# Kernel tuning notes

Hardware: AMD Instinct MI355X
Metric: run time of the kernel (lower is better)

The kernel has to match this reference:

```python
import jax, jax.numpy as jnp
import numpy as np

EMBED = 768
HEADS = 12
HEAD_DIM = EMBED // HEADS
DEPTH = 4
PATCH = 16
GRID = 32  # 512 / 16
MLP_DIM = 4 * EMBED
LN_EPS = 1e-5


def layer_norm(x, w, b):
    m = jnp.mean(x, axis=-1, keepdims=True)
    v = jnp.mean(jnp.square(x - m), axis=-1, keepdims=True)
    return (x - m) * jax.lax.rsqrt(v + LN_EPS) * w + b


def sam_attention(x, qkv_w, qkv_b, proj_w, proj_b, rel_pos_h, rel_pos_w):
    B, H, W, C = x.shape
    N = H * W
    scale = HEAD_DIM ** -0.5
    qkv = x.reshape(B, N, C) @ qkv_w + qkv_b  # (B, N, 3C)
    qkv = qkv.reshape(B, N, 3, HEADS, HEAD_DIM).transpose(2, 0, 3, 1, 4)
    qkv = qkv.reshape(3, B * HEADS, N, HEAD_DIM)
    q, k, v = qkv[0], qkv[1], qkv[2]
    attn = jnp.einsum('bqc,bkc->bqk', q * scale, k)  # (B*nh, N, N)
    # decomposed relative position (q_size == k_size, table already max_rel_dist)
    idx_h = jnp.arange(H)[:, None] - jnp.arange(H)[None, :] + (H - 1)
    idx_w = jnp.arange(W)[:, None] - jnp.arange(W)[None, :] + (W - 1)
    Rh = rel_pos_h[idx_h]  # (H, H, hd)
    Rw = rel_pos_w[idx_w]  # (W, W, hd)
    r_q = q.reshape(B * HEADS, H, W, HEAD_DIM)
    rel_h = jnp.einsum('bhwc,hkc->bhwk', r_q, Rh)
    rel_w = jnp.einsum('bhwc,wkc->bhwk', r_q, Rw)
    attn = (attn.reshape(B * HEADS, H, W, H, W)
            + rel_h[:, :, :, :, None]
            + rel_w[:, :, :, None, :]).reshape(B * HEADS, N, N)
    attn = jax.nn.softmax(attn, axis=-1)
    out = (attn @ v).reshape(B, HEADS, H, W, HEAD_DIM)
    out = out.transpose(0, 2, 3, 1, 4).reshape(B, H, W, C)
    return out @ proj_w + proj_b


def setup_inputs() -> dict:
    key = jax.random.key(0)
    ks = jax.random.split(key, 20)
    s = lambda k, shape, sc=0.02: jax.random.normal(k, shape, jnp.float32) * sc
    inp = {
        'x': jax.random.normal(ks[0], (4, 3, 512, 512), jnp.float32),
        'conv_w': s(ks[1], (EMBED, 3, PATCH, PATCH)),
        'conv_b': jnp.zeros((EMBED,), jnp.float32),
        'pos_embed': s(ks[2], (1, GRID, GRID, EMBED)),
        'ln1_w': jnp.ones((DEPTH, EMBED), jnp.float32),
        'ln1_b': jnp.zeros((DEPTH, EMBED), jnp.float32),
        'qkv_w': s(ks[3], (DEPTH, EMBED, 3 * EMBED)),
        'qkv_b': jnp.zeros((DEPTH, 3 * EMBED), jnp.float32),
        'proj_w': s(ks[4], (DEPTH, EMBED, EMBED)),
        'proj_b': jnp.zeros((DEPTH, EMBED), jnp.float32),
        'rel_pos_h': s(ks[5], (DEPTH, 2 * GRID - 1, HEAD_DIM)),
        'rel_pos_w': s(ks[6], (DEPTH, 2 * GRID - 1, HEAD_DIM)),
        'ln2_w': jnp.ones((DEPTH, EMBED), jnp.float32),
        'ln2_b': jnp.zeros((DEPTH, EMBED), jnp.float32),
        'fc1_w': s(ks[7], (DEPTH, EMBED, MLP_DIM)),
        'fc1_b': jnp.zeros((DEPTH, MLP_DIM), jnp.float32),
        'fc2_w': s(ks[8], (DEPTH, MLP_DIM, EMBED)),
        'fc2_b': jnp.zeros((DEPTH, EMBED), jnp.float32),
    }
    return inp


def reference(x, conv_w, conv_b, pos_embed, ln1_w, ln1_b, qkv_w, qkv_b,
              proj_w, proj_b, rel_pos_h, rel_pos_w, ln2_w, ln2_b,
              fc1_w, fc1_b, fc2_w, fc2_b):
    # patch embed: conv stride=patch, then NCHW -> NHWC
    h = jax.lax.conv_general_dilated(
        x, conv_w, window_strides=(PATCH, PATCH), padding='VALID',
        dimension_numbers=('NCHW', 'OIHW', 'NCHW'))
    h = h.transpose(0, 2, 3, 1) + conv_b  # (B, 32, 32, 768)
    h = h + pos_embed
    for i in range(DEPTH):
        a = sam_attention(layer_norm(h, ln1_w[i], ln1_b[i]),
                          qkv_w[i], qkv_b[i], proj_w[i], proj_b[i],
                          rel_pos_h[i], rel_pos_w[i])
        h = h + a
        m = layer_norm(h, ln2_w[i], ln2_b[i])
        m = jax.nn.gelu(m @ fc1_w[i] + fc1_b[i], approximate=False) @ fc2_w[i] + fc2_b[i]
        h = h + m
    return h
```

## Files before the change

### kernel.cpp

```cpp
#include <hip/hip_runtime.h>
#include <hip/hip_bf16.h>
#include <math.h>
#include <stdint.h>

#define EMBED 768
#define NTOK  1024
#define BATCH 4
#define NHEAD 12
#define HD    64
#define MLPD  3072
#define M_ROWS 4096

typedef __attribute__((ext_vector_type(8))) short short8;
typedef __attribute__((ext_vector_type(4))) float floatx4;

__device__ __forceinline__ float b2f(__hip_bfloat16 v) { return __bfloat162float(v); }

__device__ __forceinline__ void gld_lds16(const void* g, void* l) {
    __builtin_amdgcn_global_load_lds(
        (const __attribute__((address_space(1))) uint32_t*)g,
        (__attribute__((address_space(3))) uint32_t*)l, 16, 0, 0);
}

__device__ __forceinline__ int swz(int row, int c) { return row*64 + (((c) ^ (row & 7)) << 3); }

__global__ __launch_bounds__(256)
void im2col(const float* __restrict__ x, __hip_bfloat16* __restrict__ A)
{
    int p  = blockIdx.x;
    int b  = p >> 10;
    int n  = p & 1023;
    int gh = n >> 5, gw = n & 31;
    int tid = threadIdx.x;
    for (int i = tid; i < 768; i += 256) {
        int ci = i >> 8, r = i & 255, kh = r >> 4, kw = r & 15;
        A[(size_t)p*768 + i] = __float2bfloat16(
            x[(((size_t)b*3 + ci)*512 + (gh*16 + kh))*512 + gw*16 + kw]);
    }
}

__global__ __launch_bounds__(256)
void cvt_bf16(const float* __restrict__ in, __hip_bfloat16* __restrict__ out, int n)
{
    int i = blockIdx.x*256 + threadIdx.x;
    if (i < n) out[i] = __float2bfloat16(in[i]);
}

__global__ __launch_bounds__(256)
void layernorm_bf16(const float* __restrict__ in,
                    const float* __restrict__ w,
                    const float* __restrict__ b,
                    __hip_bfloat16* __restrict__ out)
{
    int row = blockIdx.x;
    const float* xr = in + (size_t)row*768;
    int tid = threadIdx.x;
    float v0 = xr[tid], v1 = xr[tid+256], v2 = xr[tid+512];
    float s = v0+v1+v2, ss = v0*v0+v1*v1+v2*v2;
    __shared__ float rs[256], rss[256];
    rs[tid] = s; rss[tid] = ss; __syncthreads();
    for (int o = 128; o > 0; o >>= 1) {
        if (tid < o) { rs[tid] += rs[tid+o]; rss[tid] += rss[tid+o]; }
        __syncthreads();
    }
    float mean = rs[0] * (1.f/768.f);
    float var  = rss[0] * (1.f/768.f) - mean*mean;
    float inv  = rsqrtf(var + 1e-5f);
    out[(size_t)row*768 + tid]     = __float2bfloat16((v0-mean)*inv*w[tid]     + b[tid]);
    out[(size_t)row*768 + tid+256] = __float2bfloat16((v1-mean)*inv*w[tid+256] + b[tid+256]);
    out[(size_t)row*768 + tid+512] = __float2bfloat16((v2-mean)*inv*w[tid+512] + b[tid+512]);
}

__global__ __launch_bounds__(256)
void resum_ln(float* __restrict__ h,
              const float* __restrict__ p0, const float* __restrict__ p1,
              const float* __restrict__ bias,
              const float* __restrict__ w, const float* __restrict__ b,
              __hip_bfloat16* __restrict__ out)
{
    int row = blockIdx.x;
    int tid = threadIdx.x;
    size_t base = (size_t)row*768;
    float v[3];
    float s = 0.f, ss = 0.f;
    #pragma unroll
    for (int e = 0; e < 3; ++e) {
        int i = tid + e*256;
        float val = h[base+i] + p0[base+i] + p1[base+i] + bias[i];
        h[base+i] = val;
        v[e] = val; s += val; ss += val*val;
    }
    __shared__ float rs[256], rss[256];
    rs[tid] = s; rss[tid] = ss; __syncthreads();
    for (int o = 128; o > 0; o >>= 1) {
        if (tid < o) { rs[tid] += rs[tid+o]; rss[tid] += rss[tid+o]; }
        __syncthreads();
    }
    float mean = rs[0] * (1.f/768.f);
    float var  = rss[0] * (1.f/768.f) - mean*mean;
    float inv  = rsqrtf(var + 1e-5f);
    #pragma unroll
    for (int e = 0; e < 3; ++e) {
        int i = tid + e*256;
        out[base+i] = __float2bfloat16((v[e]-mean)*inv*w[i] + b[i]);
    }
}

__global__ __launch_bounds__(256)
void resum_out(const float* __restrict__ h,
               const float* __restrict__ p0, const float* __restrict__ p1,
               const float* __restrict__ bias,
               float* __restrict__ out)
{
    int i = blockIdx.x*256 + threadIdx.x;
    out[i] = h[i] + p0[i] + p1[i] + bias[i % 768];
}

__global__ __launch_bounds__(256)
void prep_weights(const float* __restrict__ qkv_w,  const float* __restrict__ proj_w,
                  const float* __restrict__ fc1_w,  const float* __restrict__ fc2_w,
                  __hip_bfloat16* __restrict__ qkv_wt, __hip_bfloat16* __restrict__ proj_wt,
                  __hip_bfloat16* __restrict__ fc1_wt, __hip_bfloat16* __restrict__ fc2_wt)
{
    int id = blockIdx.x;
    const float* src; __hip_bfloat16* dst; int K, N, bx, by;
    if (id < 1728)      {            src = qkv_w;  dst = qkv_wt;  K = 768;  N = 2304; bx = id % 72; by = id / 72; }
    else if (id < 2304) { id -= 1728; src = proj_w; dst = proj_wt; K = 768;  N = 768;  bx = id % 24; by = id / 24; }
    else if (id < 4608) { id -= 2304; src = fc1_w;  dst = fc1_wt;  K = 768;  N = 3072; bx = id % 96; by = id / 96; }
    else                { id -= 4608; src = fc2_w;  dst = fc2_wt;  K = 3072; N = 768;  bx = id % 24; by = id / 24; }

    __shared__ float t[32][33];
    int n0 = bx*32, k0 = by*32;
    int tx = threadIdx.x & 31, ty = threadIdx.x >> 5;
    #pragma unroll
    for (int r = 0; r < 4; ++r) {
        int row = ty + r*8;
        t[row][tx] = src[(size_t)(k0+row)*N + n0 + tx];
    }
    __syncthreads();
    #pragma unroll
    for (int r = 0; r < 4; ++r) {
        int row = ty + r*8;
        dst[(size_t)(n0+row)*K + k0 + tx] = __float2bfloat16(t[tx][row]);
    }
}

__global__ __launch_bounds__(256)
void gemm64(const __hip_bfloat16* __restrict__ A,
            const __hip_bfloat16* __restrict__ Bt,
            const float* __restrict__ bias,
            const float* __restrict__ res,
            const float* __restrict__ posadd,
            float* __restrict__ Cf,
            int M, int N, int K)
{
    __shared__ __align__(16) char smem[12288];
    __hip_bfloat16* As = (__hip_bfloat16*)smem;
    __hip_bfloat16* Bs = (__hip_bfloat16*)(smem + 4096);

    const int tid  = threadIdx.x;
    const int lane = tid & 63;
    const int wid  = tid >> 6;
    const int wr   = wid >> 1;
    const int wc   = wid & 1;
    const int lr   = lane & 15;
    const int quad = lane >> 4;

    const int bm = blockIdx.y * 64;
    const int bn = blockIdx.x * 128;

    const int srow  = tid >> 2;
    const int skoff = (tid & 3) * 8;
    const int wbase = wid * 1024;

    floatx4 acc[2][4];
    #pragma unroll
    for (int i = 0; i < 2; ++i)
        #pragma unroll
        for (int j = 0; j < 4; ++j)
            acc[i][j] = (floatx4){0.f,0.f,0.f,0.f};

    for (int k0 = 0; k0 < K; k0 += 32) {
        gld_lds16(A + (size_t)(bm + srow)*K + k0 + skoff, (char*)As + wbase);
        #pragma unroll
        for (int c = 0; c < 2; ++c)
            gld_lds16(Bt + (size_t)(bn + c*64 + srow)*K + k0 + skoff,
                      (char*)Bs + c*4096 + wbase);
        __syncthreads();

        short8 a[2], b[4];
        #pragma unroll
        for (int i = 0; i < 2; ++i)
            a[i] = *(const short8*)((const void*)(As + (wr*32 + i*16 + lr)*32 + quad*8));
        #pragma unroll
        for (int j = 0; j < 4; ++j)
            b[j] = *(const short8*)((const void*)(Bs + (wc*64 + j*16 + lr)*32 + quad*8));
        #pragma unroll
        for (int i = 0; i < 2; ++i)
            #pragma unroll
            for (int j = 0; j < 4; ++j)
                acc[i][j] = __builtin_amdgcn_mfma_f32_16x16x32_bf16(a[i], b[j], acc[i][j], 0, 0, 0);
        __syncthreads();
    }

    #pragma unroll
    for (int j = 0; j < 4; ++j) {
        int col = bn + wc*64 + j*16 + lr;
        float bs = bias[col];
        #pragma unroll
        for (int i = 0; i < 2; ++i) {
            #pragma unroll
            for (int r = 0; r < 4; ++r) {
                int row = bm + wr*32 + i*16 + quad*4 + r;
                float val = acc[i][j][r] + bs;
                if (res)    val += res[(size_t)row*N + col];
                if (posadd) val += posadd[(size_t)(row & 1023)*N + col];
                Cf[(size_t)row*N + col] = val;
            }
        }
    }
}

__global__ __launch_bounds__(256)
void gemm128(const __hip_bfloat16* __restrict__ A,
             const __hip_bfloat16* __restrict__ Bt,
             const float* __restrict__ bias,
             float* __restrict__ Cf,
             __hip_bfloat16* __restrict__ Cb,
             __hip_bfloat16* __restrict__ qp,
             __hip_bfloat16* __restrict__ kp,
             __hip_bfloat16* __restrict__ vp,
             int M, int N, int K, int S, int dogelu, int emode)
{
    __shared__ __align__(16) char smem[20480];
    __hip_bfloat16* As = (__hip_bfloat16*)smem;
    __hip_bfloat16* Bs = (__hip_bfloat16*)(smem + 8192);

    const int tid  = threadIdx.x;
    const int lane = tid & 63;
    const int wid  = tid >> 6;
    const int wr   = wid >> 1;
    const int wc   = wid & 1;
    const int lr   = lane & 15;
    const int quad = lane >> 4;

    const int bm = blockIdx.y * 128;
    const int bn = blockIdx.x * 128;
    const int z  = blockIdx.z;
    const int Kseg = K / S;
    const int kbeg = z * Kseg;
    const int kend = kbeg + Kseg;

    const int srow  = tid >> 2;
    const int skoff = (tid & 3) * 8;
    const int wbase = wid * 1024;

    floatx4 acc[4][4];
    #pragma unroll
    for (int i = 0; i < 4; ++i)
        #pragma unroll
        for (int j = 0; j < 4; ++j)
            acc[i][j] = (floatx4){0.f,0.f,0.f,0.f};

    for (int k0 = kbeg; k0 < kend; k0 += 32) {
        #pragma unroll
        for (int c = 0; c < 2; ++c)
            gld_lds16(A + (size_t)(bm + c*64 + srow)*K + k0 + skoff,
                      (char*)As + c*4096 + wbase);
        #pragma unroll
        for (int c = 0; c < 2; ++c)
            gld_lds16(Bt + (size_t)(bn + c*64 + srow)*K + k0 + skoff,
                      (char*)Bs + c*4096 + wbase);
        __syncthreads();

        short8 a[4], b[4];
        #pragma unroll
        for (int i = 0; i < 4; ++i)
            a[i] = *(const short8*)((const void*)(As + (wr*64 + i*16 + lr)*32 + quad*8));
        #pragma unroll
        for (int j = 0; j < 4; ++j)
            b[j] = *(const short8*)((const void*)(Bs + (wc*64 + j*16 + lr)*32 + quad*8));
        #pragma unroll
        for (int i = 0; i < 4; ++i)
            #pragma unroll
            for (int j = 0; j < 4; ++j)
                acc[i][j] = __builtin_amdgcn_mfma_f32_16x16x32_bf16(a[i], b[j], acc[i][j], 0, 0, 0);
        __syncthreads();
    }

    if (emode == 3) {
        #pragma unroll
        for (int j = 0; j < 4; ++j) {
            int col = bn + wc*64 + j*16 + lr;
            #pragma unroll
            for (int i = 0; i < 4; ++i) {
                #pragma unroll
                for (int r = 0; r < 4; ++r) {
                    int row = bm + wr*64 + i*16 + quad*4 + r;
                    Cf[(size_t)z*M*N + (size_t)row*N + col] = acc[i][j][r];
                }
            }
        }
        return;
    }

    __hip_bfloat16* epi = (__hip_bfloat16*)(smem + wid*4864);

    if (emode == 1) {
        #pragma unroll
        for (int p = 0; p < 2; ++p) {
            #pragma unroll
            for (int j = 0; j < 4; ++j) {
                float bs = bias[bn + wc*64 + j*16 + lr];
                #pragma unroll
                for (int ii = 0; ii < 2; ++ii) {
                    int i = p*2 + ii;
                    #pragma unroll
                    for (int r = 0; r < 4; ++r) {
                        float val = acc[i][j][r] + bs;
                        if (dogelu) val = 0.5f*val*(1.f + erff(val*0.70710678118f));
                        epi[(ii*16 + quad*4 + r)*72 + j*16 + lr] = __float2bfloat16(val);
                    }
                }
            }
            #pragma unroll
            for (int p2 = 0; p2 < 4; ++p2) {
                int row = p2*8 + (lane >> 3), chunk = lane & 7;
                short8 v = *(const short8*)((const void*)(epi + row*72 + chunk*8));
                *(short8*)((void*)(Cb + (size_t)(bm + wr*64 + p*32 + row)*N
                                      + bn + wc*64 + chunk*8)) = v;
            }
        }
        return;
    }

    const int head64 = (bn + wc*64) >> 6;
    const int which  = head64 / 12;
    const int head   = head64 % 12;
    const int b_     = (bm + wr*64) >> 10;
    const int bh     = b_*NHEAD + head;
    const int n0     = (bm + wr*64) & 1023;

    if (which < 2) {
        __hip_bfloat16* dst = (which == 0 ? qp : kp) + ((size_t)bh*NTOK + n0)*HD;
        #pragma unroll
        for (int p = 0; p < 2; ++p) {
            #pragma unroll
            for (int j = 0; j < 4; ++j) {
                float bs = bias[bn + wc*64 + j*16 + lr];
                #pragma unroll
                for (int ii = 0; ii < 2; ++ii) {
                    int i = p*2 + ii;
                    #pragma unroll
                    for (int r = 0; r < 4; ++r)
                        epi[(ii*16 + quad*4 + r)*72 + j*16 + lr] =
                            __float2bfloat16(acc[i][j][r] + bs);
                }
            }
            #pragma unroll
            for (int p2 = 0; p2 < 4; ++p2) {
                int row = p2*8 + (lane >> 3), chunk = lane & 7;
                short8 v = *(const short8*)((const void*)(epi + row*72 + chunk*8));
                *(short8*)((void*)(dst + (size_t)(p*32 + row)*HD + chunk*8)) = v;
            }
        }
    } else {
        __hip_bfloat16* dstv = vp + (size_t)bh*HD*NTOK + n0;
        #pragma unroll
        for (int p = 0; p < 2; ++p) {
            #pragma unroll
            for (int j = 0; j < 4; ++j) {
                float bs = bias[bn + wc*64 + j*16 + lr];
                #pragma unroll
                for (int ii = 0; ii < 2; ++ii) {
                    int i = p*2 + ii;
                    #pragma unroll
                    for (int r = 0; r < 4; ++r)
                        epi[(j*16 + lr)*36 + ii*16 + quad*4 + r] =
                            __float2bfloat16(acc[i][j][r] + bs);
                }
            }
            #pragma unroll
            for (int p2 = 0; p2 < 4; ++p2) {
                int d = p2*16 + (lane >> 2), chunk = lane & 3;
                short8 v = *(const short8*)((const void*)(epi + d*36 + chunk*8));
                *(short8*)((void*)(dstv + (size_t)d*NTOK + p*32 + chunk*8)) = v;
            }
        }
    }
}

__global__ __launch_bounds__(256)
void attention_mfma(const __hip_bfloat16* __restrict__ qp,
                    const __hip_bfloat16* __restrict__ kp,
                    const __hip_bfloat16* __restrict__ vp,
                    const float* __restrict__ rph,
                    const float* __restrict__ rpw,
                    __hip_bfloat16* __restrict__ out)
{
    const int blk  = blockIdx.x;
    const int bh   = blk >> 4;
    const int qt   = blk & 15;
    const int b    = bh / NHEAD;
    const int head = bh % NHEAD;
    const int tid  = threadIdx.x;
    const int lane = tid & 63;
    const int w    = tid >> 6;
    const int lr   = lane & 15;
    const int quad = lane >> 4;

    __shared__ __align__(16) __hip_bfloat16 Qs[64*64];
    __shared__ __align__(16) __hip_bfloat16 Ks[64*64];
    __shared__ __align__(16) __hip_bfloat16 Vs[64*64];
    __shared__ __align__(16) __hip_bfloat16 Ps[4*16*64];
    __shared__ float relhS[64*32];
    __shared__ float relwS[64*32];

    const __hip_bfloat16* qb = qp + ((size_t)bh*NTOK + qt*64)*HD;
    const __hip_bfloat16* kb = kp + (size_t)bh*NTOK*HD;
    const __hip_bfloat16* vb = vp + (size_t)bh*HD*NTOK;

    const int sr = tid >> 2;
    const int sc = (tid & 3) * 2;

    short8 kreg0, kreg1, vreg0, vreg1;
    {
        const __hip_bfloat16* kk = kb + (size_t)sr*HD + sc*8;
        kreg0 = *(const short8*)((const void*)kk);
        kreg1 = *(const short8*)((const void*)(kk + 8));
        const __hip_bfloat16* vv = vb + (size_t)sr*NTOK + sc*8;
        vreg0 = *(const short8*)((const void*)vv);
        vreg1 = *(const short8*)((const void*)(vv + 8));
    }

    {
        const __hip_bfloat16* qq = qb + (size_t)sr*HD + sc*8;
        short8 q0 = *(const short8*)((const void*)qq);
        short8 q1 = *(const short8*)((const void*)(qq + 8));
        *(short8*)((void*)(Qs + swz(sr, sc)))   = q0;
        *(short8*)((void*)(Qs + swz(sr, sc+1))) = q1;
    }

    for (int i = tid; i < 504; i += 256) {
        int r = i >> 3, c = i & 7;
        const float* ph = rph + (size_t)r*HD + c*8;
        const float* pw = rpw + (size_t)r*HD + c*8;
        union { short8 v; __hip_bfloat16 e[8]; } uh, uw;
        #pragma unroll
        for (int e = 0; e < 8; ++e) { uh.e[e] = __float2bfloat16(ph[e]); uw.e[e] = __float2bfloat16(pw[e]); }
        *(short8*)((void*)(Ks + swz(r, c))) = uh.v;
        *(short8*)((void*)(Vs + swz(r, c))) = uw.v;
    }
    if (tid < 16) {
        short8 z = (short8){0,0,0,0,0,0,0,0};
        int c = tid & 7;
        if (tid < 8) *(short8*)((void*)(Ks + swz(63, c))) = z;
        else         *(short8*)((void*)(Vs + swz(63, c))) = z;
    }
    __syncthreads();

    short8 qa0 = *(const short8*)((const void*)(Qs + swz(w*16 + lr, quad)));
    short8 qa1 = *(const short8*)((const void*)(Qs + swz(w*16 + lr, 4 + quad)));

    const int qrow = w*16 + quad*4;
    const int qh_  = qt*2 + (w >> 1);
    const int qw_  = (w & 1)*16 + quad*4;

    #pragma unroll
    for (int j = 0; j < 4; ++j) {
        int t = j*16 + lr;
        short8 th0 = *(const short8*)((const void*)(Ks + swz(j*16 + lr, quad)));
        short8 th1 = *(const short8*)((const void*)(Ks + swz(j*16 + lr, 4 + quad)));
        floatx4 ha = (floatx4){0.f,0.f,0.f,0.f};
        ha = __builtin_amdgcn_mfma_f32_16x16x32_bf16(qa0, th0, ha, 0, 0, 0);
        ha = __builtin_amdgcn_mfma_f32_16x16x32_bf16(qa1, th1, ha, 0, 0, 0);
        short8 tw0 = *(const short8*)((const void*)(Vs + swz(j*16 + lr, quad)));
        short8 tw1 = *(const short8*)((const void*)(Vs + swz(j*16 + lr, 4 + quad)));
        floatx4 wa = (floatx4){0.f,0.f,0.f,0.f};
        wa = __builtin_amdgcn_mfma_f32_16x16x32_bf16(qa0, tw0, wa, 0, 0, 0);
        wa = __builtin_amdgcn_mfma_f32_16x16x32_bf16(qa1, tw1, wa, 0, 0, 0);
        int kh = qh_ + 31 - t;
        #pragma unroll
        for (int rr = 0; rr < 4; ++rr) {
            if (kh >= 0 && kh < 32) relhS[(qrow + rr)*32 + kh] = ha[rr];
            int kw = qw_ + rr + 31 - t;
            if (kw >= 0 && kw < 32) relwS[(qrow + rr)*32 + kw] = wa[rr];
        }
    }

    float rw[4][2];
    #pragma unroll
    for (int rr = 0; rr < 4; ++rr)
        #pragma unroll
        for (int jp = 0; jp < 2; ++jp)
            rw[rr][jp] = relwS[(qrow + rr)*32 + jp*16 + lr];

    floatx4 o[4];
    #pragma unroll
    for (int ds = 0; ds < 4; ++ds) o[ds] = (floatx4){0.f,0.f,0.f,0.f};
    float lsum[4] = {0.f, 0.f, 0.f, 0.f};

    const float scale = 0.125f;

    for (int kt = 0; kt < 16; ++kt) {
        __syncthreads();
        *(short8*)((void*)(Ks + swz(sr, sc)))   = kreg0;
        *(short8*)((void*)(Ks + swz(sr, sc+1))) = kreg1;
        *(short8*)((void*)(Vs + swz(sr, sc)))   = vreg0;
        *(short8*)((void*)(Vs + swz(sr, sc+1))) = vreg1;
        __syncthreads();

        if (kt < 15) {
            const __hip_bfloat16* kk = kb + (size_t)(kt+1)*64*HD + (size_t)sr*HD + sc*8;
            kreg0 = *(const short8*)((const void*)kk);
            kreg1 = *(const short8*)((const void*)(kk + 8));
            const __hip_bfloat16* vv = vb + (size_t)sr*NTOK + (kt+1)*64 + sc*8;
            vreg0 = *(const short8*)((const void*)vv);
            vreg1 = *(const short8*)((const void*)(vv + 8));
        }

        float2 rh2[4];
        #pragma unroll
        for (int rr = 0; rr < 4; ++rr)
            rh2[rr] = *(const float2*)((const void*)(relhS + (qrow + rr)*32 + kt*2));

        floatx4 sv[4];
        #pragma unroll
        for (int j = 0; j < 4; ++j) {
            short8 kb0 = *(const short8*)((const void*)(Ks + swz(j*16 + lr, quad)));
            short8 kb1 = *(const short8*)((const void*)(Ks + swz(j*16 + lr, 4 + quad)));
            floatx4 z = (floatx4){0.f,0.f,0.f,0.f};
            z = __builtin_amdgcn_mfma_f32_16x16x32_bf16(qa0, kb0, z, 0, 0, 0);
            z = __builtin_amdgcn_mfma_f32_16x16x32_bf16(qa1, kb1, z, 0, 0, 0);
            sv[j] = z;
        }

        #pragma unroll
        for (int j = 0; j < 4; ++j) {
            int colc = j*2 + (lr >> 3);
            #pragma unroll
            for (int rr = 0; rr < 4; ++rr) {
                float s = sv[j][rr]*scale + ((j < 2) ? rh2[rr].x : rh2[rr].y) + rw[rr][j & 1];
                s = fminf(fmaxf(s, -60.f), 60.f);
                float pp = __expf(s);
                lsum[rr] += pp;
                int prow = quad*4 + rr;
                Ps[w*1024 + prow*64 + ((colc ^ (prow & 7)) << 3) + (lr & 7)] = __float2bfloat16(pp);
            }
        }

        short8 pa0 = *(const short8*)((const void*)(Ps + w*1024 + swz(lr, quad)));
        short8 pa1 = *(const short8*)((const void*)(Ps + w*1024 + swz(lr, 4 + quad)));
        #pragma unroll
        for (int ds = 0; ds < 4; ++ds) {
            short8 v0 = *(const short8*)((const void*)(Vs + swz(ds*16 + lr, quad)));
            short8 v1 = *(const short8*)((const void*)(Vs + swz(ds*16 + lr, 4 + quad)));
            o[ds] = __builtin_amdgcn_mfma_f32_16x16x32_bf16(pa0, v0, o[ds], 0, 0, 0);
            o[ds] = __builtin_amdgcn_mfma_f32_16x16x32_bf16(pa1, v1, o[ds], 0, 0, 0);
        }
    }

    #pragma unroll
    for (int off = 1; off < 16; off <<= 1)
        #pragma unroll
        for (int rr = 0; rr < 4; ++rr)
            lsum[rr] += __shfl_xor(lsum[rr], off, 16);

    #pragma unroll
    for (int rr = 0; rr < 4; ++rr) {
        float inv = 1.f / lsum[rr];
        int n = qt*64 + w*16 + quad*4 + rr;
        size_t base = ((size_t)b*NTOK + n)*EMBED + head*HD;
        #pragma unroll
        for (int ds = 0; ds < 4; ++ds)
            out[base + ds*16 + lr] = __float2bfloat16(o[ds][rr] * inv);
    }
}

extern "C" void kernel_launch(void* const* d_in, const int* in_sizes, int n_in,
                              void* d_out, int out_size, void* d_ws, size_t ws_size,
                              hipStream_t stream)
{
    const float* x      = (const float*)d_in[0];
    const float* conv_w = (const float*)d_in[1];
    const float* conv_b = (const float*)d_in[2];
    const float* pos    = (const float*)d_in[3];
    const float* ln1_w  = (const float*)d_in[4];
    const float* ln1_b  = (const float*)d_in[5];
    const float* qkv_w  = (const float*)d_in[6];
    const float* qkv_b  = (const float*)d_in[7];
    const float* proj_w = (const float*)d_in[8];
    const float* proj_b = (const float*)d_in[9];
    const float* rph    = (const float*)d_in[10];
    const float* rpw    = (const float*)d_in[11];
    const float* ln2_w  = (const float*)d_in[12];
    const float* ln2_b  = (const float*)d_in[13];
    const float* fc1_w  = (const float*)d_in[14];
    const float* fc1_b  = (const float*)d_in[15];
    const float* fc2_w  = (const float*)d_in[16];
    const float* fc2_b  = (const float*)d_in[17];

    char* p = (char*)d_ws;
    float*           h       = (float*)p;           p += (size_t)M_ROWS*EMBED*4;
    __hip_bfloat16*  q_perm  = (__hip_bfloat16*)p;
    float*           p0      = (float*)p;           p += (size_t)48*NTOK*HD*2;
    __hip_bfloat16*  k_perm  = (__hip_bfloat16*)p;  p += (size_t)48*NTOK*HD*2;
    __hip_bfloat16*  vt_perm = (__hip_bfloat16*)p;  p += (size_t)48*NTOK*HD*2;
    __hip_bfloat16*  attn_o  = (__hip_bfloat16*)p;  p += (size_t)M_ROWS*EMBED*2;
    __hip_bfloat16*  x_ln    = (__hip_bfloat16*)p;  p += (size_t)M_ROWS*EMBED*2;
    __hip_bfloat16*  mlp     = (__hip_bfloat16*)p;  p += (size_t)M_ROWS*MLPD*2;
    __hip_bfloat16*  qkv_wt  = (__hip_bfloat16*)p;  p += (size_t)2304*768*2;
    __hip_bfloat16*  proj_wt = (__hip_bfloat16*)p;  p += (size_t)768*768*2;
    __hip_bfloat16*  fc1_wt  = (__hip_bfloat16*)p;  p += (size_t)MLPD*768*2;
    __hip_bfloat16*  fc2_wt  = (__hip_bfloat16*)p;  p += (size_t)768*MLPD*2;

    __hip_bfloat16*  A_im    = mlp;
    __hip_bfloat16*  conv_wt = qkv_wt;

    im2col<<<M_ROWS, 256, 0, stream>>>(x, A_im);
    cvt_bf16<<<(768*768 + 255)/256, 256, 0, stream>>>(conv_w, conv_wt, 768*768);
    gemm64<<<dim3(768/128, M_ROWS/64, 1), 256, 0, stream>>>(
        A_im, conv_wt, conv_b, nullptr, pos, h, M_ROWS, 768, 768);

    layernorm_bf16<<<M_ROWS, 256, 0, stream>>>(h, ln1_w, ln1_b, x_ln);

    for (int L = 0; L < 4; ++L) {
        prep_weights<<<6912, 256, 0, stream>>>(
            qkv_w + (size_t)L*768*2304, proj_w + (size_t)L*768*768,
            fc1_w + (size_t)L*768*MLPD, fc2_w + (size_t)L*MLPD*768,
            qkv_wt, proj_wt, fc1_wt, fc2_wt);

        gemm128<<<dim3(2304/128, M_ROWS/128, 1), 256, 0, stream>>>(
            x_ln, qkv_wt, qkv_b + (size_t)L*3*EMBED,
            nullptr, nullptr, q_perm, k_perm, vt_perm,
            M_ROWS, 2304, 768, 1, 0, 2);

        attention_mfma<<<48*16, 256, 0, stream>>>(
            q_perm, k_perm, vt_perm,
            rph + (size_t)L*63*64, rpw + (size_t)L*63*64, attn_o);

        gemm64<<<dim3(768/128, M_ROWS/64, 1), 256, 0, stream>>>(
            attn_o, proj_wt, proj_b + (size_t)L*EMBED, h, nullptr,
            h, M_ROWS, 768, 768);

        layernorm_bf16<<<M_ROWS, 256, 0, stream>>>(h, ln2_w + L*EMBED, ln2_b + L*EMBED, x_ln);

        gemm128<<<dim3(MLPD/128, M_ROWS/128, 1), 256, 0, stream>>>(
            x_ln, fc1_wt, fc1_b + (size_t)L*MLPD,
            nullptr, mlp, nullptr, nullptr, nullptr,
            M_ROWS, MLPD, 768, 1, 1, 1);

        gemm128<<<dim3(768/128, M_ROWS/128, 2), 256, 0, stream>>>(
            mlp, fc2_wt, nullptr,
            p0, nullptr, nullptr, nullptr, nullptr,
            M_ROWS, 768, MLPD, 2, 0, 3);

        float* p1 = p0 + (size_t)M_ROWS*768;
        if (L < 3) {
            resum_ln<<<M_ROWS, 256, 0, stream>>>(
                h, p0, p1, fc2_b + (size_t)L*EMBED,
                ln1_w + (size_t)(L+1)*EMBED, ln1_b + (size_t)(L+1)*EMBED, x_ln);
        } else {
            resum_out<<<M_ROWS*EMBED/256, 256, 0, stream>>>(
                h, p0, p1, fc2_b + (size_t)L*EMBED, (float*)d_out);
        }
    }
}
```

Measured before the change: 992.0 us.

## Double-buffer LDS tiles in GEMM kernels and remap blocks across XCDs

Both GEMM kernels now use two LDS buffers and prefetch the next K tile with global_load_lds while MFMAs run on the current tile, dropping one barrier per iteration. This is meant to hide global load latency behind compute. Block IDs are also remapped so consecutive tiles land on the same XCD, which should improve L2 reuse. The cost is double the LDS per block, which may lower occupancy.

```diff
diff --git a/kernel.cpp b/kernel.cpp
--- a/kernel.cpp
+++ b/kernel.cpp
@@ -23,6 +23,16 @@
 }
 
 __device__ __forceinline__ int swz(int row, int c) { return row*64 + (((c) ^ (row & 7)) << 3); }
+
+__device__ __forceinline__ void xcd_remap(int gx, int gy, int& bx, int& by) {
+    int id  = blockIdx.x + gx*blockIdx.y;
+    int nwg = gx*gy;
+    int q = nwg >> 3, r = nwg & 7;
+    int xcd = id & 7, idx = id >> 3;
+    int nid = (xcd < r ? xcd*(q+1) : r*(q+1) + (xcd-r)*q) + idx;
+    bx = nid % gx;
+    by = nid / gx;
+}
 
 __global__ __launch_bounds__(256)
 void im2col(const float* __restrict__ x, __hip_bfloat16* __restrict__ A)
@@ -154,9 +164,7 @@
             float* __restrict__ Cf,
             int M, int N, int K)
 {
-    __shared__ __align__(16) char smem[12288];
-    __hip_bfloat16* As = (__hip_bfloat16*)smem;
-    __hip_bfloat16* Bs = (__hip_bfloat16*)(smem + 4096);
+    __shared__ __align__(16) char smem[24576];
 
     const int tid  = threadIdx.x;
     const int lane = tid & 63;
@@ -166,8 +174,10 @@
     const int lr   = lane & 15;
     const int quad = lane >> 4;
 
-    const int bm = blockIdx.y * 64;
-    const int bn = blockIdx.x * 128;
+    int bx, by;
+    xcd_remap(gridDim.x, gridDim.y, bx, by);
+    const int bm = by * 64;
+    const int bn = bx * 128;
 
     const int srow  = tid >> 2;
     const int skoff = (tid & 3) * 8;
@@ -180,13 +190,24 @@
         for (int j = 0; j < 4; ++j)
             acc[i][j] = (floatx4){0.f,0.f,0.f,0.f};
 
-    for (int k0 = 0; k0 < K; k0 += 32) {
-        gld_lds16(A + (size_t)(bm + srow)*K + k0 + skoff, (char*)As + wbase);
+    auto stage = [&](int bq, int k0) {
+        char* base = smem + bq*12288 + wbase;
+        gld_lds16(A + (size_t)(bm + srow)*K + k0 + skoff, base);
         #pragma unroll
         for (int c = 0; c < 2; ++c)
             gld_lds16(Bt + (size_t)(bn + c*64 + srow)*K + k0 + skoff,
-                      (char*)Bs + c*4096 + wbase);
-        __syncthreads();
+                      base + 4096 + c*4096);
+    };
+
+    const int nt = K >> 5;
+    stage(0, 0);
+    __syncthreads();
+    int cur = 0;
+    for (int t = 0; t < nt; ++t) {
+        if (t + 1 < nt) stage(cur ^ 1, (t+1)*32);
+
+        const __hip_bfloat16* As = (const __hip_bfloat16*)(smem + cur*12288);
+        const __hip_bfloat16* Bs = As + 2048;
 
         short8 a[2], b[4];
         #pragma unroll
@@ -201,6 +222,7 @@
             for (int j = 0; j < 4; ++j)
                 acc[i][j] = __builtin_amdgcn_mfma_f32_16x16x32_bf16(a[i], b[j], acc[i][j], 0, 0, 0);
         __syncthreads();
+        cur ^= 1;
     }
 
     #pragma unroll
@@ -232,9 +254,7 @@
              __hip_bfloat16* __restrict__ vp,
              int M, int N, int K, int S, int dogelu, int emode)
 {
-    __shared__ __align__(16) char smem[20480];
-    __hip_bfloat16* As = (__hip_bfloat16*)smem;
-    __hip_bfloat16* Bs = (__hip_bfloat16*)(smem + 8192);
+    __shared__ __align__(16) char smem[32768];
 
     const int tid  = threadIdx.x;
     const int lane = tid & 63;
@@ -244,12 +264,13 @@
     const int lr   = lane & 15;
     const int quad = lane >> 4;
 
-    const int bm = blockIdx.y * 128;
-    const int bn = blockIdx.x * 128;
+    int bx, by;
+    xcd_remap(gridDim.x, gridDim.y, bx, by);
+    const int bm = by * 128;
+    const int bn = bx * 128;
     const int z  = blockIdx.z;
     const int Kseg = K / S;
     const int kbeg = z * Kseg;
-    const int kend = kbeg + Kseg;
 
     const int srow  = tid >> 2;
     const int skoff = (tid & 3) * 8;
@@ -262,16 +283,27 @@
         for (int j = 0; j < 4; ++j)
             acc[i][j] = (floatx4){0.f,0.f,0.f,0.f};
 
-    for (int k0 = kbeg; k0 < kend; k0 += 32) {
+    auto stage = [&](int bq, int k0) {
+        char* base = smem + bq*16384 + wbase;
         #pragma unroll
         for (int c = 0; c < 2; ++c)
             gld_lds16(A + (size_t)(bm + c*64 + srow)*K + k0 + skoff,
-                      (char*)As + c*4096 + wbase);
+                      base + c*4096);
         #pragma unroll
         for (int c = 0; c < 2; ++c)
             gld_lds16(Bt + (size_t)(bn + c*64 + srow)*K + k0 + skoff,
-                      (char*)Bs + c*4096 + wbase);
-        __syncthreads();
+                      base + 8192 + c*4096);
+    };
+
+    const int nt = Kseg >> 5;
+    stage(0, kbeg);
+    __syncthreads();
+    int cur = 0;
+    for (int t = 0; t < nt; ++t) {
+        if (t + 1 < nt) stage(cur ^ 1, kbeg + (t+1)*32);
+
+        const __hip_bfloat16* As = (const __hip_bfloat16*)(smem + cur*16384);
+        const __hip_bfloat16* Bs = As + 4096;
 
         short8 a[4], b[4];
         #pragma unroll
@@ -286,6 +318,7 @@
             for (int j = 0; j < 4; ++j)
                 acc[i][j] = __builtin_amdgcn_mfma_f32_16x16x32_bf16(a[i], b[j], acc[i][j], 0, 0, 0);
         __syncthreads();
+        cur ^= 1;
     }
 
     if (emode == 3) {
```

New measurement: 960.2 us. -3.2%, faster.
